# Kernel tuning notes

Hardware: AMD Instinct MI355X
Metric: run time of the kernel (lower is better)

Reference implementation:

```python
import jax, jax.numpy as jnp
import numpy as np

NUM_HEADS = 12


def setup_inputs() -> dict:
    key = jax.random.key(0)
    ks = jax.random.split(key, 5)
    B, N, D = 8, 1024, 768
    x = jax.random.normal(ks[0], (B, N, D), dtype=jnp.float32)
    w_qkv = jax.random.normal(ks[1], (D, 3 * D), dtype=jnp.float32) * (D ** -0.5)
    b_qkv = jax.random.normal(ks[2], (3 * D,), dtype=jnp.float32) * 0.02
    w_proj = jax.random.normal(ks[3], (D, D), dtype=jnp.float32) * (D ** -0.5)
    b_proj = jax.random.normal(ks[4], (D,), dtype=jnp.float32) * 0.02
    return {"x": x, "w_qkv": w_qkv, "b_qkv": b_qkv, "w_proj": w_proj, "b_proj": b_proj}


def reference(x, w_qkv, b_qkv, w_proj, b_proj):
    B, N, D = x.shape
    H = NUM_HEADS
    hd = D // H
    scale = hd ** -0.5
    qkv = x @ w_qkv + b_qkv                      # [B, N, 3D]
    qkv = qkv.reshape(B, N, 3, H, hd)
    q, k, v = jnp.moveaxis(qkv, 2, 0)            # each [B, N, H, hd]
    # scores: [B, H, N, N]
    scores = jnp.einsum("bqhd,bkhd->bhqk", q, k) * scale
    attn = jax.nn.softmax(scores, axis=-1)
    a = jnp.einsum("bhqk,bkhd->bqhd", attn, v)   # [B, N, H, hd]
    a = a.reshape(B, N, D)
    return a @ w_proj + b_proj
```

## Files before the change

kernel.cpp:

```cpp
#include <hip/hip_runtime.h>

#define B_ 8
#define N_ 1024
#define D_ 768
#define H_ 12
#define HD 64
#define M_ (B_*N_)

typedef short short8 __attribute__((ext_vector_type(8)));
typedef float f32x4 __attribute__((ext_vector_type(4)));
typedef float f32x16 __attribute__((ext_vector_type(16)));
typedef int int4v __attribute__((ext_vector_type(4)));

__device__ __forceinline__ unsigned short f2bf(float f) {
    union { float f; unsigned int u; } c; c.f = f;
    unsigned int u = c.u;
    unsigned int r = (u + 0x7fffu + ((u >> 16) & 1u)) >> 16;
    return (unsigned short)r;
}

__device__ __forceinline__ float exp2_hw(float x) {
    float r;
    asm("v_exp_f32 %0, %1" : "=v"(r) : "v"(x));
    return r;
}

__device__ __forceinline__ unsigned int cvtpk_bf16(float a, float b) {
    unsigned int r;
    asm("v_cvt_pk_bf16_f32 %0, %1, %2" : "=v"(r) : "v"(a), "v"(b));
    return r;
}

#define PLSWAP(a, b) asm volatile("v_permlane32_swap_b32 %0, %1" : "+&v"(a), "+&v"(b))

__device__ __forceinline__ short8 pack4(unsigned int a, unsigned int b,
                                        unsigned int c, unsigned int d) {
    union { int4v i; short8 s; } u;
    u.i = (int4v){(int)a, (int)b, (int)c, (int)d};
    return u.s;
}

__device__ __forceinline__ void gload16(const void* g, void* l) {
    __builtin_amdgcn_global_load_lds(
        (const __attribute__((address_space(1))) unsigned int*)g,
        (__attribute__((address_space(3))) unsigned int*)l, 16, 0, 0);
}


__global__ __launch_bounds__(256) void prep_kernel(
    const float* __restrict__ x, const float* __restrict__ wqkv,
    const float* __restrict__ wproj,
    unsigned short* __restrict__ xb, unsigned short* __restrict__ wqkvT,
    unsigned short* __restrict__ wprojT)
{
    int bid = blockIdx.x, tid = threadIdx.x;
    if (bid < 6144) {
        int i = bid * 256 + tid;
        float4 v = reinterpret_cast<const float4*>(x)[i];
        ushort4 o;
        o.x = f2bf(v.x); o.y = f2bf(v.y); o.z = f2bf(v.z); o.w = f2bf(v.w);
        reinterpret_cast<ushort4*>(xb)[i] = o;
    } else if (bid < 6144 + 6912) {
        int i = (bid - 6144) * 256 + tid;
        int r = i / 2304, c = i - r * 2304;
        wqkvT[c * 768 + r] = f2bf(wqkv[i]);
    } else {
        int i = (bid - 13056) * 256 + tid;
        int r = i / 768, c = i - r * 768;
        wprojT[c * 768 + r] = f2bf(wproj[i]);
    }
}


__global__ __launch_bounds__(512, 4) void gemm0_kernel(
    const unsigned short* __restrict__ A,
    const unsigned short* __restrict__ Bt,
    const float* __restrict__ bias,
    unsigned short* __restrict__ qo,
    unsigned short* __restrict__ ko,
    unsigned short* __restrict__ vo)
{
    const int K = D_;
    const int KT = K >> 5;
    __shared__ alignas(16) unsigned short As[3 * 8192];
    __shared__ alignas(16) unsigned short Bs[3 * 4096];

    int tid = threadIdx.x;
    int lane = tid & 63, w = tid >> 6;
    int wr = w >> 1, wc = w & 1;

    int m0 = blockIdx.y * 256, n0 = blockIdx.x * 128;

    int lr = lane & 15;
    int kc = lane >> 4;
    int org = (lane >> 4) * 4;

    int srA = w * 16 + (lane >> 2);
    int scA0 = (lane & 3) ^ (srA & 3);
    int srA1 = 128 + srA;
    int scA1 = (lane & 3) ^ (srA1 & 3);
    const unsigned short* gA0 = A + (size_t)(m0 + srA) * K + scA0 * 8;
    const unsigned short* gA1 = A + (size_t)(m0 + srA1) * K + scA1 * 8;
    const unsigned short* gB0 = Bt + (size_t)(n0 + srA) * K + scA0 * 8;

    f32x4 acc[4][4] = {};

#define STAGE_A(buf, k0)                                                   \
    do {                                                                   \
        gload16(gA0 + (k0), As + (buf) * 8192 + w * 512);                  \
        gload16(gA1 + (k0), As + (buf) * 8192 + 4096 + w * 512);           \
    } while (0)
#define STAGE_B(buf, k0) gload16(gB0 + (k0), Bs + (buf) * 4096 + w * 512)

    STAGE_A(0, 0); STAGE_B(0, 0);
    STAGE_A(1, 32); STAGE_B(1, 32);
    asm volatile("s_waitcnt vmcnt(3)" ::: "memory");
    __builtin_amdgcn_s_barrier();
    __builtin_amdgcn_sched_barrier(0);

    int cur = 0;
    for (int kt = 0; kt < KT; ++kt) {
        int sb = cur + 2; if (sb >= 3) sb -= 3;
        bool pf = (kt + 2 < KT);
        const unsigned short* Ab = As + cur * 8192;
        const unsigned short* Bb = Bs + cur * 4096;

        short8 af0, af1, bf[4];
        {
            int r0 = wr * 64 + lr;
            int r1 = wr * 64 + 16 + lr;
            af0 = *reinterpret_cast<const short8*>(&Ab[r0 * 32 + (kc ^ (r0 & 3)) * 8]);
            af1 = *reinterpret_cast<const short8*>(&Ab[r1 * 32 + (kc ^ (r1 & 3)) * 8]);
            #pragma unroll
            for (int ni = 0; ni < 4; ni++) {
                int rb = wc * 64 + ni * 16 + lr;
                bf[ni] = *reinterpret_cast<const short8*>(&Bb[rb * 32 + (kc ^ (rb & 3)) * 8]);
            }
        }
        if (pf) STAGE_A(sb, (kt + 2) * 32);
        __builtin_amdgcn_s_barrier();
        asm volatile("s_waitcnt lgkmcnt(0)" ::: "memory");
        __builtin_amdgcn_sched_barrier(0);
        __builtin_amdgcn_s_setprio(1);
        #pragma unroll
        for (int ni = 0; ni < 4; ni++) {
            acc[0][ni] = __builtin_amdgcn_mfma_f32_16x16x32_bf16(af0, bf[ni], acc[0][ni], 0, 0, 0);
            acc[1][ni] = __builtin_amdgcn_mfma_f32_16x16x32_bf16(af1, bf[ni], acc[1][ni], 0, 0, 0);
        }
        __builtin_amdgcn_s_setprio(0);
        __builtin_amdgcn_s_barrier();
        __builtin_amdgcn_sched_barrier(0);

        short8 af2, af3;
        {
            int r2 = wr * 64 + 32 + lr;
            int r3 = wr * 64 + 48 + lr;
            af2 = *reinterpret_cast<const short8*>(&Ab[r2 * 32 + (kc ^ (r2 & 3)) * 8]);
            af3 = *reinterpret_cast<const short8*>(&Ab[r3 * 32 + (kc ^ (r3 & 3)) * 8]);
        }
        if (pf) STAGE_B(sb, (kt + 2) * 32);
        __builtin_amdgcn_s_barrier();
        asm volatile("s_waitcnt lgkmcnt(0)" ::: "memory");
        __builtin_amdgcn_sched_barrier(0);
        __builtin_amdgcn_s_setprio(1);
        #pragma unroll
        for (int ni = 0; ni < 4; ni++) {
            acc[2][ni] = __builtin_amdgcn_mfma_f32_16x16x32_bf16(af2, bf[ni], acc[2][ni], 0, 0, 0);
            acc[3][ni] = __builtin_amdgcn_mfma_f32_16x16x32_bf16(af3, bf[ni], acc[3][ni], 0, 0, 0);
        }
        __builtin_amdgcn_s_setprio(0);
        if (kt + 1 < KT) {
            if (pf) asm volatile("s_waitcnt vmcnt(3)" ::: "memory");
            else    asm volatile("s_waitcnt vmcnt(0)" ::: "memory");
        }
        __builtin_amdgcn_s_barrier();
        __builtin_amdgcn_sched_barrier(0);

        cur = (cur == 2) ? 0 : cur + 1;
    }
#undef STAGE_A
#undef STAGE_B

    if (n0 >= 1536) {
        #pragma unroll
        for (int mi = 0; mi < 4; mi++) {
            int nn0g = m0 + wr * 64 + mi * 16 + org;
            int b = nn0g >> 10, nn = nn0g & 1023;
            #pragma unroll
            for (int ni = 0; ni < 4; ni++) {
                int colg = n0 + wc * 64 + ni * 16 + lr;
                int rem = colg - 1536;
                int h = rem >> 6, dd = rem & 63;
                float bv = bias[colg];
                unsigned long long u = 0;
                #pragma unroll
                for (int r = 0; r < 4; r++)
                    u |= (unsigned long long)f2bf(acc[mi][ni][r] + bv) << (16 * r);
                *reinterpret_cast<unsigned long long*>(
                    vo + ((size_t)(b * H_ + h) * HD + dd) * N_ + nn) = u;
            }
        }
    } else {
        int which = n0 / 768;
        unsigned short* dst = (which == 0) ? qo : ko;
        float fold = (which == 0) ? 0.125f * 1.44269504088896f : 1.0f;
        #pragma unroll
        for (int mi = 0; mi < 4; mi++) {
            #pragma unroll
            for (int ni = 0; ni < 4; ni++) {
                int col = n0 + wc * 64 + ni * 16 + lr;
                int rem = col - which * 768;
                int h = rem >> 6, dd = rem & 63;
                float bv = bias[col];
                #pragma unroll
                for (int r = 0; r < 4; r++) {
                    int row = m0 + wr * 64 + mi * 16 + org + r;
                    int b = row >> 10, nn = row & 1023;
                    dst[(((size_t)(b * H_ + h) * N_ + nn) * HD) + dd] =
                        f2bf((acc[mi][ni][r] + bv) * fold);
                }
            }
        }
    }
}


__global__ __launch_bounds__(256) void gemm1_kernel(
    const unsigned short* __restrict__ A,
    const unsigned short* __restrict__ Bt,
    const float* __restrict__ bias,
    float* __restrict__ outf,
    int Ndim, int K)
{
    __shared__ alignas(16) unsigned short As[3 * 4096];
    __shared__ alignas(16) unsigned short Bs[3 * 4096];

    int tid = threadIdx.x;
    int lane = tid & 63, w = tid >> 6;
    int wr = w >> 1, wc = w & 1;

    int nbx = Ndim >> 7;
    int nwg = gridDim.x;
    int cpx = nwg >> 3;
    int sbid = (blockIdx.x & 7) * cpx + (blockIdx.x >> 3);
    int bx = sbid % nbx, by = sbid / nbx;
    int m0 = by * 128, n0 = bx * 128;

    int lr = lane & 15, lk8 = (lane >> 4) * 8;
    int org = (lane >> 4) * 4;

    int srow = tid >> 2;
    int selem = (tid & 3) * 8;
    const unsigned short* gA = A + (size_t)(m0 + srow) * K + selem;
    const unsigned short* gB = Bt + (size_t)(n0 + srow) * K + selem;

    f32x4 acc[4][4] = {};

#define GSTAGE(buf, k0)                                                    \
    do {                                                                   \
        gload16(gA + (k0), As + (buf) * 4096 + w * 512);                   \
        gload16(gA + (size_t)64 * K + (k0), As + (buf) * 4096 + 2048 + w * 512);\
        gload16(gB + (k0), Bs + (buf) * 4096 + w * 512);                   \
        gload16(gB + (size_t)64 * K + (k0), Bs + (buf) * 4096 + 2048 + w * 512);\
    } while (0)

    GSTAGE(0, 0);
    GSTAGE(1, 32);
    asm volatile("s_waitcnt vmcnt(4)" ::: "memory");
    __builtin_amdgcn_s_barrier();
    __builtin_amdgcn_sched_barrier(0);

    int KT = K >> 5;
    int cur = 0;
    for (int kt = 0; kt < KT; ++kt) {
        int sb = cur + 2; if (sb >= 3) sb -= 3;
        if (kt + 2 < KT) GSTAGE(sb, (kt + 2) * 32);

        const unsigned short* Ab = As + cur * 4096;
        const unsigned short* Bb = Bs + cur * 4096;
        short8 af[4], bf[4];
        #pragma unroll
        for (int mi = 0; mi < 4; mi++)
            af[mi] = *reinterpret_cast<const short8*>(&Ab[(wr * 64 + mi * 16 + lr) * 32 + lk8]);
        #pragma unroll
        for (int ni = 0; ni < 4; ni++)
            bf[ni] = *reinterpret_cast<const short8*>(&Bb[(wc * 64 + ni * 16 + lr) * 32 + lk8]);
        #pragma unroll
        for (int mi = 0; mi < 4; mi++)
            #pragma unroll
            for (int ni = 0; ni < 4; ni++)
                acc[mi][ni] = __builtin_amdgcn_mfma_f32_16x16x32_bf16(bf[ni], af[mi], acc[mi][ni], 0, 0, 0);

        if (kt + 1 < KT) {
            if (kt + 2 < KT)
                asm volatile("s_waitcnt vmcnt(4)" ::: "memory");
            else
                asm volatile("s_waitcnt vmcnt(0)" ::: "memory");
            __builtin_amdgcn_s_barrier();
            __builtin_amdgcn_sched_barrier(0);
            cur = (cur == 2) ? 0 : cur + 1;
        }
    }
#undef GSTAGE

    int m = m0 + wr * 64 + lr;
    #pragma unroll
    for (int mi = 0; mi < 4; mi++) {
        int row = m + mi * 16;
        #pragma unroll
        for (int ni = 0; ni < 4; ni++) {
            int col = n0 + wc * 64 + ni * 16 + org;
            float4 bv = *reinterpret_cast<const float4*>(&bias[col]);
            float4 o;
            o.x = acc[mi][ni][0] + bv.x;
            o.y = acc[mi][ni][1] + bv.y;
            o.z = acc[mi][ni][2] + bv.z;
            o.w = acc[mi][ni][3] + bv.w;
            *reinterpret_cast<float4*>(&outf[(size_t)row * Ndim + col]) = o;
        }
    }
}


__global__ __launch_bounds__(256) void attn_kernel(
    const unsigned short* __restrict__ qg,
    const unsigned short* __restrict__ kg,
    const unsigned short* __restrict__ vtg,
    unsigned short* __restrict__ aout)
{
    __shared__ alignas(16) unsigned short Ks[2][4096];
    __shared__ alignas(16) unsigned short Vs[2][4096];

    int tid = threadIdx.x;
    int lane = tid & 63, w = tid >> 6;

    int bid = blockIdx.x;
    int xcd = bid & 7;
    int chunk = bid >> 3;
    int bh = xcd * 12 + (chunk % 12);
    int qblk = chunk / 12;
    int b = bh / H_, h = bh - b * H_;
    int q0w = qblk * 128 + w * 32;
    int l31 = lane & 31;
    int hi = lane >> 5;
    int swz = l31 & 7;

    const unsigned short* qp = qg + ((size_t)bh * N_ + q0w + l31) * HD + hi * 8;
    short8 qf[4];
    #pragma unroll
    for (int ds = 0; ds < 4; ds++)
        qf[ds] = *reinterpret_cast<const short8*>(qp + ds * 16);

    const unsigned short* kbh = kg + (size_t)bh * N_ * HD;
    const unsigned short* vtbh = vtg + (size_t)bh * HD * N_;

    int sr0 = tid >> 3;
    int sj0 = (tid & 7) ^ (sr0 & 7);
    int sr1 = sr0 + 32;
    int sj1 = (tid & 7) ^ (sr1 & 7);

    float m_run = -INFINITY, l_run = 0.f;
    f32x16 o0 = {}, o1 = {};

#define STAGE(buf, kv0)                                                        \
    do {                                                                       \
        gload16(kbh + (size_t)((kv0) + sr0) * HD + sj0 * 8, &Ks[buf][w * 512]);\
        gload16(kbh + (size_t)((kv0) + sr1) * HD + sj1 * 8, &Ks[buf][2048 + w * 512]);\
        gload16(vtbh + (size_t)sr0 * N_ + (kv0) + sj0 * 8, &Vs[buf][w * 512]); \
        gload16(vtbh + (size_t)sr1 * N_ + (kv0) + sj1 * 8, &Vs[buf][2048 + w * 512]);\
    } while (0)

    STAGE(0, 0);
    asm volatile("s_waitcnt vmcnt(0)" ::: "memory");
    __builtin_amdgcn_s_barrier();
    __builtin_amdgcn_sched_barrier(0);

    int cur = 0;
    for (int t = 0; t < 16; ++t) {
        if (t < 15) STAGE(cur ^ 1, (t + 1) * 64);

        const unsigned short* Ksb = Ks[cur];
        const unsigned short* Vsb = Vs[cur];

        f32x16 s0 = {}, s1 = {};
        #pragma unroll
        for (int ds = 0; ds < 4; ds++) {
            int pc = (ds * 2 + hi) ^ swz;
            short8 kf0 = *reinterpret_cast<const short8*>(&Ksb[(l31) * 64 + pc * 8]);
            short8 kf1 = *reinterpret_cast<const short8*>(&Ksb[(32 + l31) * 64 + pc * 8]);
            s0 = __builtin_amdgcn_mfma_f32_32x32x16_bf16(kf0, qf[ds], s0, 0, 0, 0);
            s1 = __builtin_amdgcn_mfma_f32_32x32x16_bf16(kf1, qf[ds], s1, 0, 0, 0);
        }

        float mx = s0[0];
        #pragma unroll
        for (int r = 1; r < 16; r++) mx = fmaxf(mx, s0[r]);
        #pragma unroll
        for (int r = 0; r < 16; r++) mx = fmaxf(mx, s1[r]);
        mx = fmaxf(mx, __shfl_xor(mx, 32, 64));

        if (__any(mx > m_run + 8.f)) {
            float mn = fmaxf(m_run, mx);
            float al = exp2_hw(m_run - mn);
            m_run = mn;
            l_run *= al;
            o0 *= al;
            o1 *= al;
        }

        float psum = 0.f;
        #pragma unroll
        for (int r = 0; r < 16; r++) { float p = exp2_hw(s0[r] - m_run); psum += p; s0[r] = p; }
        #pragma unroll
        for (int r = 0; r < 16; r++) { float p = exp2_hw(s1[r] - m_run); psum += p; s1[r] = p; }

        l_run += psum + __shfl_xor(psum, 32, 64);

        unsigned int c0[8], c1[8];
        #pragma unroll
        for (int i = 0; i < 8; i++) c0[i] = cvtpk_bf16(s0[2 * i], s0[2 * i + 1]);
        #pragma unroll
        for (int i = 0; i < 8; i++) c1[i] = cvtpk_bf16(s1[2 * i], s1[2 * i + 1]);
        PLSWAP(c0[0], c0[2]); PLSWAP(c0[1], c0[3]);
        PLSWAP(c0[4], c0[6]); PLSWAP(c0[5], c0[7]);
        PLSWAP(c1[0], c1[2]); PLSWAP(c1[1], c1[3]);
        PLSWAP(c1[4], c1[6]); PLSWAP(c1[5], c1[7]);
        short8 pa0 = pack4(c0[0], c0[1], c0[2], c0[3]);
        short8 pa1 = pack4(c0[4], c0[5], c0[6], c0[7]);
        short8 pa2 = pack4(c1[0], c1[1], c1[2], c1[3]);
        short8 pa3 = pack4(c1[4], c1[5], c1[6], c1[7]);

        #pragma unroll
        for (int ks = 0; ks < 4; ks++) {
            int pc = (ks * 2 + hi) ^ swz;
            short8 vf0 = *reinterpret_cast<const short8*>(&Vsb[(l31) * 64 + pc * 8]);
            short8 vf1 = *reinterpret_cast<const short8*>(&Vsb[(32 + l31) * 64 + pc * 8]);
            short8 pa = (ks == 0) ? pa0 : (ks == 1) ? pa1 : (ks == 2) ? pa2 : pa3;
            o0 = __builtin_amdgcn_mfma_f32_32x32x16_bf16(vf0, pa, o0, 0, 0, 0);
            o1 = __builtin_amdgcn_mfma_f32_32x32x16_bf16(vf1, pa, o1, 0, 0, 0);
        }

        if (t < 15) {
            asm volatile("s_waitcnt vmcnt(0)" ::: "memory");
            __builtin_amdgcn_s_barrier();
            __builtin_amdgcn_sched_barrier(0);
            cur ^= 1;
        }
    }
#undef STAGE

    float linv = 1.0f / l_run;
    unsigned short* op = aout + ((size_t)(b * N_ + q0w + l31)) * D_ + h * HD;
    #pragma unroll
    for (int rg = 0; rg < 4; rg++) {
        int dbase = 8 * rg + 4 * hi;
        unsigned long long u0 = 0, u1 = 0;
        #pragma unroll
        for (int k = 0; k < 4; k++) {
            u0 |= (unsigned long long)f2bf(o0[rg * 4 + k] * linv) << (16 * k);
            u1 |= (unsigned long long)f2bf(o1[rg * 4 + k] * linv) << (16 * k);
        }
        *reinterpret_cast<unsigned long long*>(op + dbase) = u0;
        *reinterpret_cast<unsigned long long*>(op + 32 + dbase) = u1;
    }
}


extern "C" void kernel_launch(void* const* d_in, const int* in_sizes, int n_in,
                              void* d_out, int out_size, void* d_ws, size_t ws_size,
                              hipStream_t stream) {
    const float* x      = (const float*)d_in[0];
    const float* w_qkv  = (const float*)d_in[1];
    const float* b_qkv  = (const float*)d_in[2];
    const float* w_proj = (const float*)d_in[3];
    const float* b_proj = (const float*)d_in[4];
    float* out = (float*)d_out;

    char* ws = (char*)d_ws;
    unsigned short* xb     = (unsigned short*)(ws + 0);
    unsigned short* wqkvT  = (unsigned short*)(ws + 12582912);
    unsigned short* wprojT = (unsigned short*)(ws + 16121856);
    unsigned short* qb     = (unsigned short*)(ws + 17301504);
    unsigned short* kb     = (unsigned short*)(ws + 29884416);
    unsigned short* vtb    = (unsigned short*)(ws + 42467328);
    unsigned short* aout   = xb;

    prep_kernel<<<15360, 256, 0, stream>>>(x, w_qkv, w_proj, xb, wqkvT, wprojT);

    gemm0_kernel<<<dim3(18, 32), 512, 0, stream>>>(
        xb, wqkvT, b_qkv, qb, kb, vtb);

    attn_kernel<<<768, 256, 0, stream>>>(qb, kb, vtb, aout);

    gemm1_kernel<<<384, 256, 0, stream>>>(
        aout, wprojT, b_proj, out, D_, D_);
}
```

Measured before the change: 134.8 us.

## Triple-buffer attention K/V loads, add MFMA priority, tile weight transpose via LDS

The attention kernel moves from double to triple buffering of K/V tiles in shared memory. It now prefetches two tiles ahead and waits with vmcnt(4) instead of draining all loads, so global-load latency overlaps more compute. s_setprio is raised around the MFMA sections to favour matrix-issue waves. Separately, the weight conversion and transpose in prep_kernel now goes through a 64x64 LDS tile, so reads and writes are coalesced instead of scattered 2-byte stores, and the grid shrinks to match. The extra buffers raise LDS use per block, which may reduce occupancy.

```diff
diff --git a/kernel.cpp b/kernel.cpp
--- a/kernel.cpp
+++ b/kernel.cpp
@@ -60,14 +60,37 @@
         ushort4 o;
         o.x = f2bf(v.x); o.y = f2bf(v.y); o.z = f2bf(v.z); o.w = f2bf(v.w);
         reinterpret_cast<ushort4*>(xb)[i] = o;
-    } else if (bid < 6144 + 6912) {
-        int i = (bid - 6144) * 256 + tid;
-        int r = i / 2304, c = i - r * 2304;
-        wqkvT[c * 768 + r] = f2bf(wqkv[i]);
-    } else {
-        int i = (bid - 13056) * 256 + tid;
-        int r = i / 768, c = i - r * 768;
-        wprojT[c * 768 + r] = f2bf(wproj[i]);
+        return;
+    }
+    __shared__ unsigned short T[64][72];
+    const float* W; unsigned short* wT; int Rr, Cc, idx;
+    if (bid < 6144 + 432) { W = wqkv;  wT = wqkvT;  Rr = 768; Cc = 2304; idx = bid - 6144; }
+    else                  { W = wproj; wT = wprojT; Rr = 768; Cc = 768;  idx = bid - 6576; }
+    int ntc = Cc >> 6;
+    int tc = idx % ntc, tr = idx / ntc;
+    int r0 = tr * 64, c0 = tc * 64;
+    {
+        int row = tid >> 2, cg = (tid & 3) * 16;
+        const float4* src = reinterpret_cast<const float4*>(&W[(size_t)(r0 + row) * Cc + c0 + cg]);
+        ushort4 o[4];
+        #pragma unroll
+        for (int j = 0; j < 4; j++) {
+            float4 v = src[j];
+            o[j].x = f2bf(v.x); o[j].y = f2bf(v.y); o[j].z = f2bf(v.z); o[j].w = f2bf(v.w);
+        }
+        #pragma unroll
+        for (int j = 0; j < 4; j++)
+            *reinterpret_cast<ushort4*>(&T[row][cg + j * 4]) = o[j];
+    }
+    __syncthreads();
+    {
+        int orow = tid >> 2, rg = (tid & 3) * 16;
+        unsigned short tmp[16];
+        #pragma unroll
+        for (int j = 0; j < 16; j++) tmp[j] = T[rg + j][orow];
+        uint4* dst = reinterpret_cast<uint4*>(&wT[(size_t)(c0 + orow) * Rr + r0 + rg]);
+        dst[0] = *reinterpret_cast<const uint4*>(&tmp[0]);
+        dst[1] = *reinterpret_cast<const uint4*>(&tmp[8]);
     }
 }
 
@@ -328,8 +351,8 @@
     const unsigned short* __restrict__ vtg,
     unsigned short* __restrict__ aout)
 {
-    __shared__ alignas(16) unsigned short Ks[2][4096];
-    __shared__ alignas(16) unsigned short Vs[2][4096];
+    __shared__ alignas(16) unsigned short Ks[3][4096];
+    __shared__ alignas(16) unsigned short Vs[3][4096];
 
     int tid = threadIdx.x;
     int lane = tid & 63, w = tid >> 6;
@@ -371,18 +394,22 @@
     } while (0)
 
     STAGE(0, 0);
-    asm volatile("s_waitcnt vmcnt(0)" ::: "memory");
+    STAGE(1, 64);
+    asm volatile("s_waitcnt vmcnt(4)" ::: "memory");
     __builtin_amdgcn_s_barrier();
     __builtin_amdgcn_sched_barrier(0);
 
     int cur = 0;
     for (int t = 0; t < 16; ++t) {
-        if (t < 15) STAGE(cur ^ 1, (t + 1) * 64);
+        int sb = cur + 2; if (sb >= 3) sb -= 3;
+        bool pf = (t + 2 < 16);
+        if (pf) STAGE(sb, (t + 2) * 64);
 
         const unsigned short* Ksb = Ks[cur];
         const unsigned short* Vsb = Vs[cur];
 
         f32x16 s0 = {}, s1 = {};
+        __builtin_amdgcn_s_setprio(1);
         #pragma unroll
         for (int ds = 0; ds < 4; ds++) {
             int pc = (ds * 2 + hi) ^ swz;
@@ -391,6 +418,7 @@
             s0 = __builtin_amdgcn_mfma_f32_32x32x16_bf16(kf0, qf[ds], s0, 0, 0, 0);
             s1 = __builtin_amdgcn_mfma_f32_32x32x16_bf16(kf1, qf[ds], s1, 0, 0, 0);
         }
+        __builtin_amdgcn_s_setprio(0);
 
         float mx = s0[0];
         #pragma unroll
@@ -430,6 +458,7 @@
         short8 pa2 = pack4(c1[0], c1[1], c1[2], c1[3]);
         short8 pa3 = pack4(c1[4], c1[5], c1[6], c1[7]);
 
+        __builtin_amdgcn_s_setprio(1);
         #pragma unroll
         for (int ks = 0; ks < 4; ks++) {
             int pc = (ks * 2 + hi) ^ swz;
@@ -439,12 +468,14 @@
             o0 = __builtin_amdgcn_mfma_f32_32x32x16_bf16(vf0, pa, o0, 0, 0, 0);
             o1 = __builtin_amdgcn_mfma_f32_32x32x16_bf16(vf1, pa, o1, 0, 0, 0);
         }
+        __builtin_amdgcn_s_setprio(0);
 
         if (t < 15) {
-            asm volatile("s_waitcnt vmcnt(0)" ::: "memory");
+            if (pf) asm volatile("s_waitcnt vmcnt(4)" ::: "memory");
+            else    asm volatile("s_waitcnt vmcnt(0)" ::: "memory");
             __builtin_amdgcn_s_barrier();
             __builtin_amdgcn_sched_barrier(0);
-            cur ^= 1;
+            cur = (cur == 2) ? 0 : cur + 1;
         }
     }
 #undef STAGE
@@ -485,7 +516,7 @@
     unsigned short* vtb    = (unsigned short*)(ws + 42467328);
     unsigned short* aout   = xb;
 
-    prep_kernel<<<15360, 256, 0, stream>>>(x, w_qkv, w_proj, xb, wqkvT, wprojT);
+    prep_kernel<<<6720, 256, 0, stream>>>(x, w_qkv, w_proj, xb, wqkvT, wprojT);
 
     gemm0_kernel<<<dim3(18, 32), 512, 0, stream>>>(
         xb, wqkvT, b_qkv, qb, kb, vtb);
```

Result: faster. 128.0 us (-5.0%).
